# Kernel tuning notes

Hardware: AMD Instinct MI355X
Metric: run time of the kernel (lower is better)

Reference implementation:

```python
import jax, jax.numpy as jnp
import numpy as np

N_QUBITS = 9   # kernelsize**2
N_LAYERS = 2   # BasicEntanglerLayers depth
KS = 3
FILTERS = 4


def _rx(theta):
    # RX(theta) = [[cos(t/2), -i sin(t/2)], [-i sin(t/2), cos(t/2)]]
    c = jnp.cos(theta / 2).astype(jnp.complex64)
    s = (-1j) * jnp.sin(theta / 2).astype(jnp.complex64)
    return jnp.stack([jnp.stack([c, s]), jnp.stack([s, c])])


def _apply_1q(state, gate, wire):
    # state: (2,)*N_QUBITS complex64
    s = jnp.moveaxis(state, wire, 0).reshape(2, -1)
    s = gate @ s
    return jnp.moveaxis(s.reshape((2,) * N_QUBITS), 0, wire)


def _apply_cnot(state, c, t):
    s0 = jnp.take(state, 0, axis=c)
    s1 = jnp.take(state, 1, axis=c)
    ft = t if t < c else t - 1  # target axis index after removing control axis
    s1 = jnp.flip(s1, axis=ft)
    return jnp.stack([s0, s1], axis=c)


def _circuit(p, w):
    # p: (N_QUBITS,) input angles; w: (N_LAYERS, N_QUBITS) trainable angles
    state = jnp.zeros((2,) * N_QUBITS, dtype=jnp.complex64).at[(0,) * N_QUBITS].set(1.0)
    # AngleEmbedding (rotation='X', PennyLane default)
    for i in range(N_QUBITS):
        state = _apply_1q(state, _rx(p[i]), i)
    # BasicEntanglerLayers: RX rotations + CNOT ring per layer
    for l in range(N_LAYERS):
        for i in range(N_QUBITS):
            state = _apply_1q(state, _rx(w[l, i]), i)
        for i in range(N_QUBITS):
            state = _apply_cnot(state, i, (i + 1) % N_QUBITS)
    probs = state.real ** 2 + state.imag ** 2
    z = []
    for i in range(N_QUBITS):
        pi = probs.sum(axis=tuple(a for a in range(N_QUBITS) if a != i))  # (2,)
        z.append(pi[0] - pi[1])  # <Z_i>
    return jnp.stack(z)  # (N_QUBITS,)


def setup_inputs() -> dict:
    key = jax.random.key(0)
    k1, k2 = jax.random.split(key)
    x = jax.random.normal(k1, (4, 3, 28, 28), dtype=jnp.float32)
    qweights = jax.random.uniform(k2, (N_LAYERS, N_QUBITS), dtype=jnp.float32, minval=0.0, maxval=2.0 * np.pi)
    return {"x": x, "qweights": qweights}


def reference(x, qweights):
    B, C, H, W = x.shape
    h_out = H - KS + 1
    w_out = W - KS + 1
    # Patch extraction: (B, C, h_out, w_out, KS*KS)
    patches = jnp.stack(
        [x[:, :, dy:dy + h_out, dx:dx + w_out] for dy in range(KS) for dx in range(KS)],
        axis=-1,
    )
    # With stride=1 the overlapping scatter writes in the original are fully
    # overwritten by later iterations, so out[b,f,y,x,c] == circuit(patch)[f].
    q = jax.vmap(_circuit, in_axes=(0, None))(patches.reshape(-1, KS * KS), qweights)
    q = q.reshape(B, C, h_out, w_out, N_QUBITS)[..., :FILTERS]
    out = q.mean(axis=1)  # mean over channels -> (B, h_out, w_out, F)
    return jnp.transpose(out, (0, 3, 1, 2))  # (B, F, h_out, w_out)
```

## Files before the change

### kernel.cpp

```cpp
#include <hip/hip_runtime.h>


static constexpr int CH = 3;
static constexpr int HOUT = 26;
static constexpr int WOUT = 26;
static constexpr int NPIX = 4 * HOUT * WOUT;

__global__ __launch_bounds__(64) void quanv_closed(
    const float* __restrict__ x,
    const float* __restrict__ w,
    float* __restrict__ out)
{
  const int pix = blockIdx.x * 64 + threadIdx.x;
  if (pix >= NPIX) return;
  const int b  = pix / (HOUT * WOUT);
  const int r  = pix % (HOUT * WOUT);
  const int oy = r / WOUT;
  const int ox = r % WOUT;

  float cw[9], sw[9];
#pragma unroll
  for (int q = 0; q < 9; ++q) __sincosf(w[9 + q], &sw[q], &cw[q]);

  const float CC01 = cw[0] * cw[1], SS01 = sw[0] * sw[1];
  const float CC12 = cw[1] * cw[2], SS12 = sw[1] * sw[2];
  const float CC23 = cw[2] * cw[3], SS23 = sw[2] * sw[3];
  const float CC45 = cw[4] * cw[5], SS45 = sw[4] * sw[5];
  const float CC67 = cw[6] * cw[7], SS67 = sw[6] * sw[7];
  const float C18  = cw[1] * cw[8];

  const float W000 =  C18 * CC23 * CC45 * CC67;
  const float W100 =  C18 * SS23 * CC45 * CC67;
  const float W010 =  C18 * CC23 * SS45 * CC67;
  const float W001 =  C18 * CC23 * CC45 * SS67;
  const float W110 = -C18 * SS23 * SS45 * CC67;
  const float W101 =  C18 * SS23 * CC45 * SS67;
  const float W011 = -C18 * CC23 * SS45 * SS67;
  const float W111 =  C18 * SS23 * SS45 * SS67;

  const float K2a = cw[0] * CC12, K2b = cw[0] * SS12;
  const float K300 =  CC01 * CC23, K310 = SS01 * CC23;
  const float K301 =  CC01 * SS23, K311 = -SS01 * SS23;

  float acc0 = 0.f, acc1 = 0.f, acc2 = 0.f, acc3 = 0.f;

#pragma unroll
  for (int ch = 0; ch < CH; ++ch) {
    float cf[9], sf[9];
#pragma unroll
    for (int i = 0; i < 9; ++i) {
      const int dy = i / 3, dx = i % 3;
      const float p = x[((b * CH + ch) * 28 + (oy + dy)) * 28 + (ox + dx)];
      __sincosf(p + w[i], &sf[i], &cf[i]);
    }

    acc0 += W000 * cf[2] * cf[4] * cf[6] * cf[8]
          + W100 * sf[2] * sf[4] * cf[6] * cf[8]
          + W010 * cf[2] * sf[4] * sf[6] * cf[8]
          + W001 * cf[2] * cf[4] * sf[6] * sf[8]
          + W110 * sf[2] * cf[4] * sf[6] * cf[8]
          + W101 * sf[2] * sf[4] * sf[6] * sf[8]
          + W011 * cf[2] * sf[4] * cf[6] * sf[8]
          + W111 * sf[2] * cf[4] * cf[6] * sf[8];

    const float c5678  = cf[5] * cf[6] * cf[7] * cf[8];
    const float c45678 = cf[4] * c5678;

    acc1 += cf[3] * c45678 * (CC01 * cf[0] * cf[2] + SS01 * sf[0] * sf[2]);

    acc2 += c45678 * (K2a * cf[1] * cf[3] + K2b * sf[1] * sf[3]);

    acc3 += c5678 * (K300 * cf[0] * cf[2] * cf[4]
                   + K310 * sf[0] * sf[2] * cf[4]
                   + K301 * cf[0] * sf[2] * sf[4]
                   + K311 * sf[0] * cf[2] * sf[4]);
  }

  const float inv3 = 1.f / 3.f;
  out[((b * 4 + 0) * HOUT + oy) * WOUT + ox] = acc0 * inv3;
  out[((b * 4 + 1) * HOUT + oy) * WOUT + ox] = acc1 * inv3;
  out[((b * 4 + 2) * HOUT + oy) * WOUT + ox] = acc2 * inv3;
  out[((b * 4 + 3) * HOUT + oy) * WOUT + ox] = acc3 * inv3;
}

extern "C" void kernel_launch(void* const* d_in, const int* in_sizes, int n_in,
                              void* d_out, int out_size, void* d_ws, size_t ws_size,
                              hipStream_t stream) {
  const float* x = (const float*)d_in[0];
  const float* w = (const float*)d_in[1];
  float* out = (float*)d_out;
  dim3 grid((NPIX + 63) / 64);
  dim3 block(64);
  hipLaunchKernelGGL(quanv_closed, grid, block, 0, stream, x, w, out);
}
```

Baseline: 56.11 us.

## Split channels across threads and reduce through shared memory

Each block now runs 192 threads, one wavefront per input channel, so each thread evaluates a single channel's circuit expectations instead of looping over all three. The per-channel results go to LDS and are averaged after a __syncthreads by the first wavefront, which writes the output. This triples thread-level parallelism for a tiny grid that could not fill the GPU, at the cost of recomputing the weight trig per thread, a barrier, and shared-memory traffic.

```diff
diff --git a/kernel.cpp b/kernel.cpp
--- a/kernel.cpp
+++ b/kernel.cpp
@@ -5,18 +5,31 @@
 static constexpr int HOUT = 26;
 static constexpr int WOUT = 26;
 static constexpr int NPIX = 4 * HOUT * WOUT;
+static constexpr int PPB = 64;
 
-__global__ __launch_bounds__(64) void quanv_closed(
+__global__ __launch_bounds__(192) void quanv_closed(
     const float* __restrict__ x,
     const float* __restrict__ w,
     float* __restrict__ out)
 {
-  const int pix = blockIdx.x * 64 + threadIdx.x;
-  if (pix >= NPIX) return;
+  __shared__ float sm[CH][PPB][4];
+
+  const int lane = threadIdx.x & 63;
+  const int ch   = threadIdx.x >> 6;
+  int pix = blockIdx.x * PPB + lane;
+  const bool valid = pix < NPIX;
+  if (!valid) pix = NPIX - 1;
   const int b  = pix / (HOUT * WOUT);
   const int r  = pix % (HOUT * WOUT);
   const int oy = r / WOUT;
   const int ox = r % WOUT;
+
+  float phi[9];
+#pragma unroll
+  for (int i = 0; i < 9; ++i) {
+    const int dy = i / 3, dx = i % 3;
+    phi[i] = x[((b * CH + ch) * 28 + (oy + dy)) * 28 + (ox + dx)] + w[i];
+  }
 
   float cw[9], sw[9];
 #pragma unroll
@@ -42,45 +55,43 @@
   const float K300 =  CC01 * CC23, K310 = SS01 * CC23;
   const float K301 =  CC01 * SS23, K311 = -SS01 * SS23;
 
-  float acc0 = 0.f, acc1 = 0.f, acc2 = 0.f, acc3 = 0.f;
+  float cf[9], sf[9];
+#pragma unroll
+  for (int i = 0; i < 9; ++i) __sincosf(phi[i], &sf[i], &cf[i]);
 
+  const float z0 = W000 * cf[2] * cf[4] * cf[6] * cf[8]
+                 + W100 * sf[2] * sf[4] * cf[6] * cf[8]
+                 + W010 * cf[2] * sf[4] * sf[6] * cf[8]
+                 + W001 * cf[2] * cf[4] * sf[6] * sf[8]
+                 + W110 * sf[2] * cf[4] * sf[6] * cf[8]
+                 + W101 * sf[2] * sf[4] * sf[6] * sf[8]
+                 + W011 * cf[2] * sf[4] * cf[6] * sf[8]
+                 + W111 * sf[2] * cf[4] * cf[6] * sf[8];
+
+  const float c5678  = cf[5] * cf[6] * cf[7] * cf[8];
+  const float c45678 = cf[4] * c5678;
+
+  const float z1 = cf[3] * c45678 * (CC01 * cf[0] * cf[2] + SS01 * sf[0] * sf[2]);
+  const float z2 = c45678 * (K2a * cf[1] * cf[3] + K2b * sf[1] * sf[3]);
+  const float z3 = c5678 * (K300 * cf[0] * cf[2] * cf[4]
+                          + K310 * sf[0] * sf[2] * cf[4]
+                          + K301 * cf[0] * sf[2] * sf[4]
+                          + K311 * sf[0] * cf[2] * sf[4]);
+
+  sm[ch][lane][0] = z0;
+  sm[ch][lane][1] = z1;
+  sm[ch][lane][2] = z2;
+  sm[ch][lane][3] = z3;
+  __syncthreads();
+
+  if (threadIdx.x < PPB && valid) {
+    const float inv3 = 1.f / 3.f;
 #pragma unroll
-  for (int ch = 0; ch < CH; ++ch) {
-    float cf[9], sf[9];
-#pragma unroll
-    for (int i = 0; i < 9; ++i) {
-      const int dy = i / 3, dx = i % 3;
-      const float p = x[((b * CH + ch) * 28 + (oy + dy)) * 28 + (ox + dx)];
-      __sincosf(p + w[i], &sf[i], &cf[i]);
+    for (int f = 0; f < 4; ++f) {
+      const float v = (sm[0][lane][f] + sm[1][lane][f] + sm[2][lane][f]) * inv3;
+      out[((b * 4 + f) * HOUT + oy) * WOUT + ox] = v;
     }
-
-    acc0 += W000 * cf[2] * cf[4] * cf[6] * cf[8]
-          + W100 * sf[2] * sf[4] * cf[6] * cf[8]
-          + W010 * cf[2] * sf[4] * sf[6] * cf[8]
-          + W001 * cf[2] * cf[4] * sf[6] * sf[8]
-          + W110 * sf[2] * cf[4] * sf[6] * cf[8]
-          + W101 * sf[2] * sf[4] * sf[6] * sf[8]
-          + W011 * cf[2] * sf[4] * cf[6] * sf[8]
-          + W111 * sf[2] * cf[4] * cf[6] * sf[8];
-
-    const float c5678  = cf[5] * cf[6] * cf[7] * cf[8];
-    const float c45678 = cf[4] * c5678;
-
-    acc1 += cf[3] * c45678 * (CC01 * cf[0] * cf[2] + SS01 * sf[0] * sf[2]);
-
-    acc2 += c45678 * (K2a * cf[1] * cf[3] + K2b * sf[1] * sf[3]);
-
-    acc3 += c5678 * (K300 * cf[0] * cf[2] * cf[4]
-                   + K310 * sf[0] * sf[2] * cf[4]
-                   + K301 * cf[0] * sf[2] * sf[4]
-                   + K311 * sf[0] * cf[2] * sf[4]);
   }
-
-  const float inv3 = 1.f / 3.f;
-  out[((b * 4 + 0) * HOUT + oy) * WOUT + ox] = acc0 * inv3;
-  out[((b * 4 + 1) * HOUT + oy) * WOUT + ox] = acc1 * inv3;
-  out[((b * 4 + 2) * HOUT + oy) * WOUT + ox] = acc2 * inv3;
-  out[((b * 4 + 3) * HOUT + oy) * WOUT + ox] = acc3 * inv3;
 }
 
 extern "C" void kernel_launch(void* const* d_in, const int* in_sizes, int n_in,
@@ -89,7 +100,7 @@
   const float* x = (const float*)d_in[0];
   const float* w = (const float*)d_in[1];
   float* out = (float*)d_out;
-  dim3 grid((NPIX + 63) / 64);
-  dim3 block(64);
+  dim3 grid((NPIX + PPB - 1) / PPB);
+  dim3 block(192);
   hipLaunchKernelGGL(quanv_closed, grid, block, 0, stream, x, w, out);
 }
```

Measured after the change: 55.36 us. No clear change (-1.3%).
